# Performance work log

Hardware: AMD Instinct MI355X
Metric: run time of the kernel (lower is better)

## Reference

```python
import jax, jax.numpy as jnp
import numpy as np

V = 49152      # HEALPix nside=64 pixel count
B = 2
FIN = 32
FOUT = 64
K = 8          # Chebyshev kernel_size
DEG = 8        # neighbors per pixel (plus self-loop -> 9 nnz/row)
G = 8          # GroupNorm num_groups
EPS = 1e-5
SLOPE = 0.1    # LeakyReLU negative slope


def setup_inputs() -> dict:
    key = jax.random.key(0)
    ks = jax.random.split(key, 4)
    rng = np.random.default_rng(0)
    # sparse Laplacian in COO: 8 random neighbors + self-loop per node
    row = np.repeat(np.arange(V, dtype=np.int32), DEG + 1)
    nbrs = rng.integers(0, V, size=(V, DEG))
    col = np.concatenate([nbrs, np.arange(V)[:, None]], axis=1).astype(np.int32).reshape(-1)
    vals = (rng.standard_normal(V * (DEG + 1)).astype(np.float32)) * 0.1
    x = jax.random.normal(ks[0], (B, V, FIN), dtype=jnp.float32)
    W1 = jax.random.normal(ks[1], (K, FIN, FOUT), dtype=jnp.float32) * 0.05
    W2 = jax.random.normal(ks[2], (K, FOUT, FOUT), dtype=jnp.float32) * 0.05
    Wr = jax.random.normal(ks[3], (K, FIN, FOUT), dtype=jnp.float32) * 0.05
    zeros = jnp.zeros((FOUT,), dtype=jnp.float32)
    ones = jnp.ones((FOUT,), dtype=jnp.float32)
    return {
        "x": x,
        "lap_vals": jnp.asarray(vals),
        "lap_row": jnp.asarray(row),
        "lap_col": jnp.asarray(col),
        "W1": W1, "b1": zeros, "g1": ones, "be1": zeros,
        "W2": W2, "b2": zeros, "g2": ones, "be2": zeros,
        "Wr": Wr, "br": zeros,
    }


def _spmm(vals, row, col, z):
    # L @ z for COO Laplacian; z: [V, D]
    return jax.ops.segment_sum(vals[:, None] * z[col], row, num_segments=V)


def _cheb_conv(x, vals, row, col, W, b):
    # x: [B, V, Fin], W: [K, Fin, Fout] -> [B, V, Fout]
    Bb, Vv, F = x.shape
    x0 = jnp.transpose(x, (1, 0, 2)).reshape(Vv, Bb * F)  # [V, B*F]
    xs = [x0, _spmm(vals, row, col, x0)]
    for _ in range(K - 2):
        xs.append(2.0 * _spmm(vals, row, col, xs[-1]) - xs[-2])
    Xk = jnp.stack(xs, 0).reshape(K, Vv, Bb, F)
    Xk = jnp.transpose(Xk, (2, 1, 0, 3))  # [B, V, K, F]
    return jnp.einsum('bvkf,kfo->bvo', Xk, W) + b


def _group_norm(x, gamma, beta):
    # equivalent to nn.GroupNorm applied on x.permute(0,2,1): normalize over (C/G, V)
    Bb, Vv, C = x.shape
    xg = x.reshape(Bb, Vv, G, C // G)
    mu = xg.mean(axis=(1, 3), keepdims=True)
    var = xg.var(axis=(1, 3), keepdims=True)
    xn = ((xg - mu) * jax.lax.rsqrt(var + EPS)).reshape(Bb, Vv, C)
    return xn * gamma + beta


def _block(x, vals, row, col, W, b, gamma, beta):
    h = _cheb_conv(x, vals, row, col, W, b)
    h = _group_norm(h, gamma, beta)
    return jax.nn.leaky_relu(h, SLOPE)  # out_channels > 1 -> LeakyReLU(0.1)


def reference(x, lap_vals, lap_row, lap_col, W1, b1, g1, be1, W2, b2, g2, be2, Wr, br):
    h = _block(x, lap_vals, lap_row, lap_col, W1, b1, g1, be1)
    h = _block(h, lap_vals, lap_row, lap_col, W2, b2, g2, be2)
    res = _cheb_conv(x, lap_vals, lap_row, lap_col, Wr, br)  # in != out -> res_conv
    return h + res
```

## Files before the change

kernel.cpp:

```cpp
#include <hip/hip_runtime.h>
#include <hip/hip_bf16.h>

#define V 49152
#define NNZ 9
#define EPSV 1e-5f
#define SLOPE 0.1f

typedef __attribute__((ext_vector_type(8))) short bf16x8;
typedef __attribute__((ext_vector_type(4))) float f32x4;

__device__ __forceinline__ float lo2f(unsigned u) { return __uint_as_float(u << 16); }
__device__ __forceinline__ float hi2f(unsigned u) { return __uint_as_float(u & 0xffff0000u); }
__device__ __forceinline__ unsigned short f2us(float f) {
    __hip_bfloat16 h = __float2bfloat16(f);
    return *(unsigned short*)&h;
}
__device__ __forceinline__ float us2f(unsigned short u) { return __uint_as_float(((unsigned)u) << 16); }
__device__ __forceinline__ unsigned pk2(float a, float b) {
    return ((unsigned)f2us(a)) | (((unsigned)f2us(b)) << 16);
}

__device__ __forceinline__ void gload_lds16(const void* g, void* l) {
    __builtin_amdgcn_global_load_lds((__attribute__((address_space(1))) void*)g,
                                     (__attribute__((address_space(3))) void*)l, 16, 0, 0);
}

__global__ __launch_bounds__(256) void prep_k(
    const float* __restrict__ W1, const float* __restrict__ Wr, const float* __restrict__ W2,
    unsigned short* __restrict__ Wt1, unsigned short* __restrict__ Wtr, unsigned short* __restrict__ Wt2,
    float* __restrict__ part)
{
    int i = blockIdx.x * 256 + threadIdx.x;
    if (i < 32768) {
        int kk = i >> 12, rem = i & 4095, o = rem >> 6, f = rem & 63;
        Wt2[i] = f2us(W2[kk * 4096 + f * 64 + o]);
    } else if (i < 49152) {
        int j = i - 32768;
        int kk = j >> 11, rem = j & 2047, o = rem >> 5, f = rem & 31;
        Wt1[j] = f2us(W1[kk * 2048 + f * 64 + o]);
    } else if (i < 65536) {
        int j = i - 49152;
        int kk = j >> 11, rem = j & 2047, o = rem >> 5, f = rem & 31;
        Wtr[j] = f2us(Wr[kk * 2048 + f * 64 + o]);
    } else if (i < 66560) {
        part[i - 65536] = 0.f;
    }
}

__global__ __launch_bounds__(256) void reorder_k(const float* __restrict__ x, unsigned* __restrict__ t0) {
    int idx = blockIdx.x * 256 + threadIdx.x;
    int v = idx >> 5, j2 = idx & 31;
    int b = j2 >> 4, f0 = (j2 & 15) * 2;
    const float* p = x + ((size_t)b * V + v) * 32 + f0;
    t0[idx] = pk2(p[0], p[1]);
}

template<int THR, bool FIRST>
__global__ __launch_bounds__(256) void spmm_step(
    const uint4* __restrict__ zc, const uint4* __restrict__ zp, uint4* __restrict__ zn,
    const float* __restrict__ vals, const int* __restrict__ col)
{
    constexpr int L4 = THR * 2;
    int tid = blockIdx.x * 256 + threadIdx.x;
    int v = tid / THR;
    int c = (tid - v * THR) * 2;
    int base = v * NNZ;
    float t[16];
    #pragma unroll
    for (int i = 0; i < 16; ++i) t[i] = 0.f;
    #pragma unroll
    for (int n = 0; n < NNZ; ++n) {
        float a = vals[base + n];
        int cc = col[base + n];
        const uint4* p = zc + (size_t)cc * L4 + c;
        uint4 u0 = p[0];
        uint4 u1 = p[1];
        t[0] += a * lo2f(u0.x); t[1] += a * hi2f(u0.x);
        t[2] += a * lo2f(u0.y); t[3] += a * hi2f(u0.y);
        t[4] += a * lo2f(u0.z); t[5] += a * hi2f(u0.z);
        t[6] += a * lo2f(u0.w); t[7] += a * hi2f(u0.w);
        t[8]  += a * lo2f(u1.x); t[9]  += a * hi2f(u1.x);
        t[10] += a * lo2f(u1.y); t[11] += a * hi2f(u1.y);
        t[12] += a * lo2f(u1.z); t[13] += a * hi2f(u1.z);
        t[14] += a * lo2f(u1.w); t[15] += a * hi2f(u1.w);
    }
    if (!FIRST) {
        const uint4* pp = zp + (size_t)v * L4 + c;
        uint4 p0 = pp[0];
        uint4 p1 = pp[1];
        t[0] = 2.f*t[0] - lo2f(p0.x); t[1] = 2.f*t[1] - hi2f(p0.x);
        t[2] = 2.f*t[2] - lo2f(p0.y); t[3] = 2.f*t[3] - hi2f(p0.y);
        t[4] = 2.f*t[4] - lo2f(p0.z); t[5] = 2.f*t[5] - hi2f(p0.z);
        t[6] = 2.f*t[6] - lo2f(p0.w); t[7] = 2.f*t[7] - hi2f(p0.w);
        t[8]  = 2.f*t[8]  - lo2f(p1.x); t[9]  = 2.f*t[9]  - hi2f(p1.x);
        t[10] = 2.f*t[10] - lo2f(p1.y); t[11] = 2.f*t[11] - hi2f(p1.y);
        t[12] = 2.f*t[12] - lo2f(p1.z); t[13] = 2.f*t[13] - hi2f(p1.z);
        t[14] = 2.f*t[14] - lo2f(p1.w); t[15] = 2.f*t[15] - hi2f(p1.w);
    }
    uint4 r0, r1;
    r0.x = pk2(t[0], t[1]);  r0.y = pk2(t[2], t[3]);
    r0.z = pk2(t[4], t[5]);  r0.w = pk2(t[6], t[7]);
    r1.x = pk2(t[8], t[9]);  r1.y = pk2(t[10], t[11]);
    r1.z = pk2(t[12], t[13]); r1.w = pk2(t[14], t[15]);
    uint4* q = zn + (size_t)v * L4 + c;
    q[0] = r0;
    q[1] = r1;
}

template<int F, int NKK, int NPH, bool DUAL, bool INIT, bool FINAL>
__global__ __launch_bounds__(256) void mfma_gemm(
    const unsigned short* __restrict__ T,
    const unsigned short* __restrict__ WtA, const unsigned short* __restrict__ WtB,
    const float* __restrict__ biasA, const float* __restrict__ biasB,
    unsigned short* __restrict__ ACC, float* __restrict__ resOut,
    float* __restrict__ part)
{
    constexpr int KPP = NKK / NPH;
    constexpr int CPR = F / 4;
    constexpr int FH = F / 32;
    constexpr int RST = 68;
    constexpr int STAGE_SH = KPP * 64 * 2 * F;
    constexpr int TRANS_SH = (DUAL ? 2 : 1) * 2 * 64 * RST * 2;
    constexpr int SH = STAGE_SH > TRANS_SH ? STAGE_SH : TRANS_SH;
    __shared__ unsigned short shraw[SH];
    __shared__ float sGrp[32];

    unsigned short* tile = shraw;
    float* accbuf  = (float*)shraw;
    float* dualbuf = accbuf + 2 * 64 * RST;

    int wv = threadIdx.x >> 6, lane = threadIdx.x & 63;
    int quad = lane >> 4, l15 = lane & 15;
    int v0 = blockIdx.x * 64;
    int ot = wv;

    bf16x8 bw[NKK][FH];
    bf16x8 bd[NKK][FH];
    f32x4 acc[4][2];
    f32x4 accd[4][2];

    #pragma unroll
    for (int ph = 0; ph < NPH; ++ph) {
        if (ph > 0) __syncthreads();

        #pragma unroll
        for (int i = 0; i < (KPP * 64 * CPR) / 256; ++i) {
            int s = (i * 4 + wv) * 64 + lane;
            int kkl = s / (64 * CPR);
            int ws = s - kkl * 64 * CPR;
            int row = ws / CPR;
            int cl = ws - row * CPR;
            int cg = (cl & ~7) | ((cl & 7) ^ (row & 7));
            const unsigned short* gp =
                T + ((size_t)(ph * KPP + kkl) * V + v0 + row) * (2 * F) + cg * 8;
            gload_lds16(gp, tile + (size_t)(i * 4 + wv) * 64 * 8);
        }

        if (ph == 0) {
            #pragma unroll
            for (int kk = 0; kk < NKK; ++kk) {
                #pragma unroll
                for (int fh = 0; fh < FH; ++fh) {
                    size_t brow = ((size_t)kk * 64 + ot * 16 + l15) * F + fh * 32 + quad * 8;
                    bw[kk][fh] = *(const bf16x8*)(const void*)(WtA + brow);
                    if constexpr (DUAL) bd[kk][fh] = *(const bf16x8*)(const void*)(WtB + brow);
                }
            }
            #pragma unroll
            for (int m = 0; m < 4; ++m)
                #pragma unroll
                for (int b = 0; b < 2; ++b) {
                    acc[m][b] = (f32x4){0.f, 0.f, 0.f, 0.f};
                    if constexpr (DUAL) accd[m][b] = (f32x4){0.f, 0.f, 0.f, 0.f};
                }
        }

        __syncthreads();

        #pragma unroll
        for (int kkl = 0; kkl < KPP; ++kkl) {
            int kk = ph * KPP + kkl;
            #pragma unroll
            for (int fh = 0; fh < FH; ++fh) {
                #pragma unroll
                for (int m = 0; m < 4; ++m) {
                    int r = m * 16 + l15;
                    int rx = r & 7;
                    const unsigned short* rbase = tile + ((size_t)kkl * 64 + r) * 2 * F;
                    #pragma unroll
                    for (int b = 0; b < 2; ++b) {
                        int c0 = b * (CPR / 2) + fh * 4 + quad;
                        int s0 = (c0 & ~7) | ((c0 & 7) ^ rx);
                        bf16x8 a = *(const bf16x8*)(const void*)(rbase + s0 * 8);
                        acc[m][b] = __builtin_amdgcn_mfma_f32_16x16x32_bf16(a, bw[kk][fh], acc[m][b], 0, 0, 0);
                        if constexpr (DUAL)
                            accd[m][b] = __builtin_amdgcn_mfma_f32_16x16x32_bf16(a, bd[kk][fh], accd[m][b], 0, 0, 0);
                    }
                }
            }
        }
    }

    __syncthreads();

    int o = ot * 16 + l15;
    float bia = FINAL ? biasA[o] : 0.f;
    float biaB = DUAL ? biasB[o] : 0.f;
    #pragma unroll
    for (int m = 0; m < 4; ++m) {
        #pragma unroll
        for (int b = 0; b < 2; ++b) {
            #pragma unroll
            for (int rr = 0; rr < 4; ++rr) {
                int r = m * 16 + quad * 4 + rr;
                accbuf[(b * 64 + r) * RST + o] = acc[m][b][rr] + bia;
                if constexpr (DUAL) dualbuf[(b * 64 + r) * RST + o] = accd[m][b][rr] + biaB;
            }
        }
    }
    if constexpr (FINAL) {
        if (threadIdx.x < 32) sGrp[threadIdx.x] = 0.f;
    }
    __syncthreads();

    #pragma unroll
    for (int j = 0; j < 4; ++j) {
        int cid = threadIdx.x + 256 * j;
        int g = cid & 7, r = (cid >> 3) & 63, b = cid >> 9;
        int o0 = g * 8;
        const float* src = accbuf + (b * 64 + r) * RST + o0;
        float e[8];
        #pragma unroll
        for (int i = 0; i < 8; ++i) e[i] = src[i];
        size_t gidx = ((size_t)b * V + v0 + r) * 64 + o0;
        if constexpr (!INIT) {
            uint4 old = *(const uint4*)(const void*)(ACC + gidx);
            e[0] += lo2f(old.x); e[1] += hi2f(old.x);
            e[2] += lo2f(old.y); e[3] += hi2f(old.y);
            e[4] += lo2f(old.z); e[5] += hi2f(old.z);
            e[6] += lo2f(old.w); e[7] += hi2f(old.w);
        }
        uint4 pk;
        pk.x = pk2(e[0], e[1]); pk.y = pk2(e[2], e[3]);
        pk.z = pk2(e[4], e[5]); pk.w = pk2(e[6], e[7]);
        *(uint4*)(void*)(ACC + gidx) = pk;
        if constexpr (FINAL) {
            float s = 0.f, q = 0.f;
            #pragma unroll
            for (int i = 0; i < 8; ++i) { s += e[i]; q += e[i] * e[i]; }
            atomicAdd(&sGrp[b * 8 + g], s);
            atomicAdd(&sGrp[16 + b * 8 + g], q);
        }
    }
    if constexpr (DUAL) {
        #pragma unroll
        for (int j = 0; j < 8; ++j) {
            int cid = threadIdx.x + 256 * j;
            int oc = cid & 15, r = (cid >> 4) & 63, b = cid >> 10;
            float4 vv = *(const float4*)(const void*)(dualbuf + (b * 64 + r) * RST + oc * 4);
            *(float4*)(void*)(resOut + ((size_t)b * V + v0 + r) * 64 + oc * 4) = vv;
        }
    }
    if constexpr (FINAL) {
        __syncthreads();
        if (threadIdx.x < 16) {
            atomicAdd(&part[threadIdx.x * 2],     sGrp[threadIdx.x]);
            atomicAdd(&part[threadIdx.x * 2 + 1], sGrp[16 + threadIdx.x]);
        }
    }
}

__global__ __launch_bounds__(256) void gn_apply(const unsigned short* __restrict__ ACC,
                                                const float* __restrict__ part,
                                                const float* __restrict__ gamma, const float* __restrict__ beta,
                                                unsigned* __restrict__ zout) {
    int idx = blockIdx.x * 256 + threadIdx.x;
    int v = idx >> 4, j = idx & 15;
    int b = j >> 3, g = j & 7;
    const float N = (float)V * 8.f;
    float mean = part[j * 2] / N;
    float rstd = rsqrtf(part[j * 2 + 1] / N - mean * mean + EPSV);
    int o0 = g * 8;
    uint4 aa = *(const uint4*)(const void*)(ACC + ((size_t)b * V + v) * 64 + o0);
    float e[8] = { lo2f(aa.x), hi2f(aa.x), lo2f(aa.y), hi2f(aa.y),
                   lo2f(aa.z), hi2f(aa.z), lo2f(aa.w), hi2f(aa.w) };
    float y[8];
    #pragma unroll
    for (int i = 0; i < 8; ++i) {
        float t = (e[i] - mean) * rstd * gamma[o0 + i] + beta[o0 + i];
        y[i] = t > 0.f ? t : SLOPE * t;
    }
    uint4 pk;
    pk.x = pk2(y[0], y[1]); pk.y = pk2(y[2], y[3]);
    pk.z = pk2(y[4], y[5]); pk.w = pk2(y[6], y[7]);
    *(uint4*)(void*)(zout + (size_t)v * 64 + b * 32 + g * 4) = pk;
}

__global__ __launch_bounds__(256) void final_out(const unsigned short* __restrict__ ACC,
                                                 float* outres,
                                                 const float* __restrict__ part,
                                                 const float* __restrict__ gamma, const float* __restrict__ beta) {
    int idx = blockIdx.x * 256 + threadIdx.x;
    int b = idx >= V * 8 ? 1 : 0;
    int r = idx - b * V * 8;
    int v = r >> 3, g = r & 7;
    int j = b * 8 + g;
    const float N = (float)V * 8.f;
    float mean = part[j * 2] / N;
    float rstd = rsqrtf(part[j * 2 + 1] / N - mean * mean + EPSV);
    int o0 = g * 8;
    size_t base = ((size_t)b * V + v) * 64 + o0;
    uint4 aa = *(const uint4*)(const void*)(ACC + base);
    float e[8] = { lo2f(aa.x), hi2f(aa.x), lo2f(aa.y), hi2f(aa.y),
                   lo2f(aa.z), hi2f(aa.z), lo2f(aa.w), hi2f(aa.w) };
    float4 r0 = *(const float4*)(const void*)(outres + base);
    float4 r1 = *(const float4*)(const void*)(outres + base + 4);
    float y[8];
    #pragma unroll
    for (int i = 0; i < 8; ++i) {
        float t = (e[i] - mean) * rstd * gamma[o0 + i] + beta[o0 + i];
        y[i] = t > 0.f ? t : SLOPE * t;
    }
    float4 w0 = { y[0] + r0.x, y[1] + r0.y, y[2] + r0.z, y[3] + r0.w };
    float4 w1 = { y[4] + r1.x, y[5] + r1.y, y[6] + r1.z, y[7] + r1.w };
    *(float4*)(void*)(outres + base) = w0;
    *(float4*)(void*)(outres + base + 4) = w1;
}

extern "C" void kernel_launch(void* const* d_in, const int* in_sizes, int n_in,
                              void* d_out, int out_size, void* d_ws, size_t ws_size,
                              hipStream_t stream) {
    const float* x    = (const float*)d_in[0];
    const float* vals = (const float*)d_in[1];
    const int*   col  = (const int*)d_in[3];
    const float* W1   = (const float*)d_in[4];
    const float* b1   = (const float*)d_in[5];
    const float* g1   = (const float*)d_in[6];
    const float* be1  = (const float*)d_in[7];
    const float* W2   = (const float*)d_in[8];
    const float* b2   = (const float*)d_in[9];
    const float* g2   = (const float*)d_in[10];
    const float* be2  = (const float*)d_in[11];
    const float* Wr   = (const float*)d_in[12];
    const float* br   = (const float*)d_in[13];
    float* out = (float*)d_out;

    unsigned short* TS  = (unsigned short*)d_ws;
    unsigned short* ACC = TS + (size_t)8 * V * 128;
    unsigned short* Wt1 = ACC + (size_t)2 * V * 64;
    unsigned short* Wtr = Wt1 + 8 * 64 * 32;
    unsigned short* Wt2 = Wtr + 8 * 64 * 32;
    float* PART1 = (float*)(Wt2 + 8 * 64 * 64);
    float* PART2 = PART1 + 32;

    prep_k<<<260, 256, 0, stream>>>(W1, Wr, W2, Wt1, Wtr, Wt2, PART1);

    uint4* T1s[8];
    for (int k = 0; k < 8; ++k) T1s[k] = (uint4*)(TS + (size_t)k * V * 64);

    reorder_k<<<V * 32 / 256, 256, 0, stream>>>(x, (unsigned*)T1s[0]);
    spmm_step<4, true><<<V * 4 / 256, 256, 0, stream>>>(T1s[0], nullptr, T1s[1], vals, col);
    for (int k = 2; k < 8; ++k)
        spmm_step<4, false><<<V * 4 / 256, 256, 0, stream>>>(T1s[k-1], T1s[k-2], T1s[k], vals, col);

    mfma_gemm<32, 8, 1, true, true, true><<<V / 64, 256, 0, stream>>>(
        TS, Wt1, Wtr, b1, br, ACC, out, PART1);

    uint4* T2s[8];
    for (int k = 0; k < 8; ++k) T2s[k] = (uint4*)(TS + (size_t)k * V * 128);

    gn_apply<<<V * 16 / 256, 256, 0, stream>>>(ACC, PART1, g1, be1, (unsigned*)T2s[0]);
    spmm_step<8, true><<<V * 8 / 256, 256, 0, stream>>>(T2s[0], nullptr, T2s[1], vals, col);
    for (int k = 2; k < 8; ++k)
        spmm_step<8, false><<<V * 8 / 256, 256, 0, stream>>>(T2s[k-1], T2s[k-2], T2s[k], vals, col);

    mfma_gemm<64, 8, 2, false, true, true><<<V / 64, 256, 0, stream>>>(
        TS, Wt2, nullptr, b2, nullptr, ACC, nullptr, PART2);

    final_out<<<2 * V * 8 / 256, 256, 0, stream>>>(ACC, out, PART2, g2, be2);
}
```

Measured before the change: 364.7 us.

## Fuse Chebyshev recurrence, GEMM and GroupNorm into two persistent cooperative kernels

Replaces the per-step SpMM launches, the separate MFMA GEMMs and the GroupNorm/output kernels with two cooperative persistent kernels (768 blocks of 64 vertices). Each block computes its rows of every Chebyshev term, keeps the tile in LDS and accumulates the MFMA product immediately, using grid.sync between terms instead of kernel boundaries. The last term is no longer written to global memory and the previous term is read from LDS. It also fuses the GroupNorm apply and residual add into the second chain. The cost is a grid-wide barrier per step and reliance on 3 blocks per CU co-residency; the old launch path is kept as a fallback.

```diff
diff --git a/kernel.cpp b/kernel.cpp
--- a/kernel.cpp
+++ b/kernel.cpp
@@ -1,10 +1,15 @@
 #include <hip/hip_runtime.h>
 #include <hip/hip_bf16.h>
+#include <hip/hip_cooperative_groups.h>
+
+namespace cg = cooperative_groups;
 
 #define V 49152
 #define NNZ 9
 #define EPSV 1e-5f
 #define SLOPE 0.1f
+#define NB 768
+#define RST 68
 
 typedef __attribute__((ext_vector_type(8))) short bf16x8;
 typedef __attribute__((ext_vector_type(4))) float f32x4;
@@ -15,11 +20,27 @@
     __hip_bfloat16 h = __float2bfloat16(f);
     return *(unsigned short*)&h;
 }
-__device__ __forceinline__ float us2f(unsigned short u) { return __uint_as_float(((unsigned)u) << 16); }
 __device__ __forceinline__ unsigned pk2(float a, float b) {
     return ((unsigned)f2us(a)) | (((unsigned)f2us(b)) << 16);
 }
-
+__device__ __forceinline__ void fma8(float* t, float a, uint4 u) {
+    t[0] += a * lo2f(u.x); t[1] += a * hi2f(u.x);
+    t[2] += a * lo2f(u.y); t[3] += a * hi2f(u.y);
+    t[4] += a * lo2f(u.z); t[5] += a * hi2f(u.z);
+    t[6] += a * lo2f(u.w); t[7] += a * hi2f(u.w);
+}
+__device__ __forceinline__ void fold8(float* t, uint4 p) {
+    t[0] = 2.f*t[0] - lo2f(p.x); t[1] = 2.f*t[1] - hi2f(p.x);
+    t[2] = 2.f*t[2] - lo2f(p.y); t[3] = 2.f*t[3] - hi2f(p.y);
+    t[4] = 2.f*t[4] - lo2f(p.z); t[5] = 2.f*t[5] - hi2f(p.z);
+    t[6] = 2.f*t[6] - lo2f(p.w); t[7] = 2.f*t[7] - hi2f(p.w);
+}
+__device__ __forceinline__ uint4 pack8(const float* t) {
+    uint4 r;
+    r.x = pk2(t[0], t[1]); r.y = pk2(t[2], t[3]);
+    r.z = pk2(t[4], t[5]); r.w = pk2(t[6], t[7]);
+    return r;
+}
 __device__ __forceinline__ void gload_lds16(const void* g, void* l) {
     __builtin_amdgcn_global_load_lds((__attribute__((address_space(1))) void*)g,
                                      (__attribute__((address_space(3))) void*)l, 16, 0, 0);
@@ -47,6 +68,344 @@
     }
 }
 
+
+__global__ __launch_bounds__(256, 3) void chain1_k(
+    const float* __restrict__ x, const float* __restrict__ vals, const int* __restrict__ col,
+    unsigned short* __restrict__ TS,
+    const unsigned short* __restrict__ Wt1, const unsigned short* __restrict__ Wtr,
+    const float* __restrict__ biasA, const float* __restrict__ biasB,
+    unsigned short* __restrict__ ACC, float* __restrict__ resOut, float* __restrict__ part)
+{
+    cg::grid_group grid = cg::this_grid();
+    __shared__ __align__(16) float epi[2 * 64 * RST];
+    __shared__ float sGrp[32];
+    uint4* tiles = (uint4*)epi;
+
+    const int tid = threadIdx.x;
+    const int wv = tid >> 6, lane = tid & 63;
+    const int quad = lane >> 4, l15 = lane & 15;
+    const int ot = wv;
+    const int v0 = blockIdx.x * 64;
+    const int sr = tid >> 2, sc2 = (tid & 3) * 2;
+    const int sv = v0 + sr;
+
+    f32x4 acc[4][2], accd[4][2];
+    #pragma unroll
+    for (int m = 0; m < 4; ++m)
+        #pragma unroll
+        for (int b = 0; b < 2; ++b) {
+            acc[m][b]  = (f32x4){0.f, 0.f, 0.f, 0.f};
+            accd[m][b] = (f32x4){0.f, 0.f, 0.f, 0.f};
+        }
+
+    auto do_mfma = [&](int kk, const unsigned short* tile_sh) {
+        size_t brow = ((size_t)kk * 64 + ot * 16 + l15) * 32 + quad * 8;
+        bf16x8 bw = *(const bf16x8*)(const void*)(Wt1 + brow);
+        bf16x8 bd = *(const bf16x8*)(const void*)(Wtr + brow);
+        #pragma unroll
+        for (int m = 0; m < 4; ++m) {
+            int r = m * 16 + l15, r7 = r & 7;
+            const unsigned short* rb = tile_sh + (size_t)r * 64;
+            #pragma unroll
+            for (int b = 0; b < 2; ++b) {
+                int s0 = (b * 4 + quad) ^ r7;
+                bf16x8 a = *(const bf16x8*)(const void*)(rb + s0 * 8);
+                acc[m][b]  = __builtin_amdgcn_mfma_f32_16x16x32_bf16(a, bw, acc[m][b], 0, 0, 0);
+                accd[m][b] = __builtin_amdgcn_mfma_f32_16x16x32_bf16(a, bd, accd[m][b], 0, 0, 0);
+            }
+        }
+    };
+
+    #pragma unroll
+    for (int j = 0; j < 2; ++j) {
+        int cid = tid + 256 * j;
+        int r = cid >> 3, c = cid & 7;
+        int b = c >> 2, f0 = (c & 3) * 8;
+        const float* p = x + ((size_t)b * V + v0 + r) * 32 + f0;
+        float4 a0 = *(const float4*)(const void*)p;
+        float4 a1 = *(const float4*)(const void*)(p + 4);
+        uint4 pk;
+        pk.x = pk2(a0.x, a0.y); pk.y = pk2(a0.z, a0.w);
+        pk.z = pk2(a1.x, a1.y); pk.w = pk2(a1.z, a1.w);
+        *(uint4*)(void*)(TS + (size_t)(v0 + r) * 64 + c * 8) = pk;
+        tiles[r * 8 + (c ^ (r & 7))] = pk;
+    }
+    __syncthreads();
+    do_mfma(0, (const unsigned short*)tiles);
+    __threadfence();
+    grid.sync();
+    __threadfence();
+
+    for (int k = 1; k < 8; ++k) {
+        const unsigned short* zc = TS + (size_t)(k - 1) * V * 64;
+        unsigned short* zn = TS + (size_t)k * V * 64;
+        uint4* bufW = tiles + (k & 1) * 512;
+        float t[16];
+        #pragma unroll
+        for (int i = 0; i < 16; ++i) t[i] = 0.f;
+        int base = sv * NNZ;
+        #pragma unroll
+        for (int n = 0; n < NNZ; ++n) {
+            float a = vals[base + n];
+            int cc = col[base + n];
+            const uint4* p = (const uint4*)(const void*)(zc + (size_t)cc * 64 + sc2 * 8);
+            fma8(t, a, p[0]);
+            fma8(t + 8, a, p[1]);
+        }
+        int s0 = sc2 ^ (sr & 7), s1 = (sc2 + 1) ^ (sr & 7);
+        if (k >= 2) {
+            fold8(t,     bufW[sr * 8 + s0]);
+            fold8(t + 8, bufW[sr * 8 + s1]);
+        }
+        uint4 r0 = pack8(t), r1 = pack8(t + 8);
+        if (k < 7) {
+            uint4* q = (uint4*)(void*)(zn + (size_t)sv * 64 + sc2 * 8);
+            q[0] = r0; q[1] = r1;
+        }
+        bufW[sr * 8 + s0] = r0;
+        bufW[sr * 8 + s1] = r1;
+        __syncthreads();
+        do_mfma(k, (const unsigned short*)bufW);
+        if (k < 7) { __threadfence(); grid.sync(); __threadfence(); }
+    }
+
+    __syncthreads();
+    int o = ot * 16 + l15;
+    float biA = biasA[o], biB = biasB[o];
+    #pragma unroll
+    for (int m = 0; m < 4; ++m)
+        #pragma unroll
+        for (int b = 0; b < 2; ++b)
+            #pragma unroll
+            for (int rr = 0; rr < 4; ++rr) {
+                int r = m * 16 + quad * 4 + rr;
+                epi[(b * 64 + r) * RST + o] = acc[m][b][rr] + biA;
+            }
+    if (tid < 32) sGrp[tid] = 0.f;
+    __syncthreads();
+    #pragma unroll
+    for (int j = 0; j < 4; ++j) {
+        int cid = tid + 256 * j;
+        int g = cid & 7, r = (cid >> 3) & 63, b = cid >> 9;
+        const float* src = epi + (b * 64 + r) * RST + g * 8;
+        float e[8], s = 0.f, q = 0.f;
+        #pragma unroll
+        for (int i = 0; i < 8; ++i) { e[i] = src[i]; s += e[i]; q += e[i] * e[i]; }
+        *(uint4*)(void*)(ACC + ((size_t)b * V + v0 + r) * 64 + g * 8) = pack8(e);
+        atomicAdd(&sGrp[b * 8 + g], s);
+        atomicAdd(&sGrp[16 + b * 8 + g], q);
+    }
+    __syncthreads();
+    #pragma unroll
+    for (int m = 0; m < 4; ++m)
+        #pragma unroll
+        for (int b = 0; b < 2; ++b)
+            #pragma unroll
+            for (int rr = 0; rr < 4; ++rr) {
+                int r = m * 16 + quad * 4 + rr;
+                epi[(b * 64 + r) * RST + o] = accd[m][b][rr] + biB;
+            }
+    __syncthreads();
+    #pragma unroll
+    for (int j = 0; j < 8; ++j) {
+        int cid = tid + 256 * j;
+        int oc = cid & 15, r = (cid >> 4) & 63, b = cid >> 10;
+        float4 vv = *(const float4*)(const void*)(epi + (b * 64 + r) * RST + oc * 4);
+        *(float4*)(void*)(resOut + ((size_t)b * V + v0 + r) * 64 + oc * 4) = vv;
+    }
+    if (tid < 16) {
+        atomicAdd(&part[tid * 2],     sGrp[tid]);
+        atomicAdd(&part[tid * 2 + 1], sGrp[16 + tid]);
+    }
+}
+
+__global__ __launch_bounds__(256, 3) void chain2_k(
+    const unsigned short* __restrict__ ACC, const float* __restrict__ part1,
+    const float* __restrict__ g1, const float* __restrict__ be1,
+    unsigned short* __restrict__ TS, const unsigned short* __restrict__ Wt2,
+    const float* __restrict__ biasA, float* __restrict__ part2,
+    const float* __restrict__ g2, const float* __restrict__ be2,
+    float* __restrict__ outres,
+    const float* __restrict__ vals, const int* __restrict__ col)
+{
+    cg::grid_group grid = cg::this_grid();
+    __shared__ __align__(16) float epi[2 * 64 * RST];
+    __shared__ float sGrp[32];
+    uint4* tiles = (uint4*)epi;
+
+    const int tid = threadIdx.x;
+    const int wv = tid >> 6, lane = tid & 63;
+    const int quad = lane >> 4, l15 = lane & 15;
+    const int ot = wv;
+    const int v0 = blockIdx.x * 64;
+    const int sr = tid >> 2, sc2 = (tid & 3) * 2;
+    const int sv = v0 + sr;
+    const float Nf = (float)V * 8.f;
+
+    f32x4 acc[4][2];
+    #pragma unroll
+    for (int m = 0; m < 4; ++m)
+        #pragma unroll
+        for (int b = 0; b < 2; ++b) acc[m][b] = (f32x4){0.f, 0.f, 0.f, 0.f};
+
+    auto do_mfma = [&](int kk, const unsigned short* tile_sh) {
+        size_t brow = ((size_t)kk * 64 + ot * 16 + l15) * 64 + quad * 8;
+        bf16x8 bw0 = *(const bf16x8*)(const void*)(Wt2 + brow);
+        bf16x8 bw1 = *(const bf16x8*)(const void*)(Wt2 + brow + 32);
+        #pragma unroll
+        for (int m = 0; m < 4; ++m) {
+            int r = m * 16 + l15, r7 = r & 7;
+            const unsigned short* rb = tile_sh + (size_t)r * 128;
+            #pragma unroll
+            for (int b = 0; b < 2; ++b) {
+                #pragma unroll
+                for (int fh = 0; fh < 2; ++fh) {
+                    int c0 = b * 8 + fh * 4 + quad;
+                    int s0 = (c0 & ~7) | ((c0 & 7) ^ r7);
+                    bf16x8 a = *(const bf16x8*)(const void*)(rb + s0 * 8);
+                    acc[m][b] = __builtin_amdgcn_mfma_f32_16x16x32_bf16(
+                        a, fh ? bw1 : bw0, acc[m][b], 0, 0, 0);
+                }
+            }
+        }
+    };
+
+    {
+        int cl = tid & 15;
+        int b = cl >> 3, g = cl & 7, j8 = b * 8 + g;
+        float mean = part1[j8 * 2] / Nf;
+        float rstd = rsqrtf(part1[j8 * 2 + 1] / Nf - mean * mean + EPSV);
+        int o0 = g * 8;
+        float gm[8], bt[8];
+        #pragma unroll
+        for (int i = 0; i < 8; ++i) { gm[i] = g1[o0 + i]; bt[i] = be1[o0 + i]; }
+        #pragma unroll
+        for (int j = 0; j < 4; ++j) {
+            int r = (tid >> 4) + 16 * j;
+            int v = v0 + r;
+            uint4 aa = *(const uint4*)(const void*)(ACC + ((size_t)b * V + v) * 64 + o0);
+            float e[8] = { lo2f(aa.x), hi2f(aa.x), lo2f(aa.y), hi2f(aa.y),
+                           lo2f(aa.z), hi2f(aa.z), lo2f(aa.w), hi2f(aa.w) };
+            float y[8];
+            #pragma unroll
+            for (int i = 0; i < 8; ++i) {
+                float t = (e[i] - mean) * rstd * gm[i] + bt[i];
+                y[i] = t > 0.f ? t : SLOPE * t;
+            }
+            uint4 pk = pack8(y);
+            *(uint4*)(void*)(TS + (size_t)v * 128 + cl * 8) = pk;
+            tiles[r * 16 + ((cl & ~7) | ((cl & 7) ^ (r & 7)))] = pk;
+        }
+    }
+    __syncthreads();
+    do_mfma(0, (const unsigned short*)tiles);
+    __threadfence();
+    grid.sync();
+    __threadfence();
+
+    for (int k = 1; k < 8; ++k) {
+        const unsigned short* zc = TS + (size_t)(k - 1) * V * 128;
+        unsigned short* zn = TS + (size_t)k * V * 128;
+        uint4* bufW = tiles + (k & 1) * 1024;
+        int base = sv * NNZ;
+        float av[NNZ]; int ac[NNZ];
+        #pragma unroll
+        for (int n = 0; n < NNZ; ++n) { av[n] = vals[base + n]; ac[n] = col[base + n]; }
+        #pragma unroll
+        for (int h = 0; h < 2; ++h) {
+            int c = h * 8 + sc2;
+            float t[16];
+            #pragma unroll
+            for (int i = 0; i < 16; ++i) t[i] = 0.f;
+            #pragma unroll
+            for (int n = 0; n < NNZ; ++n) {
+                const uint4* p = (const uint4*)(const void*)(zc + (size_t)ac[n] * 128 + c * 8);
+                fma8(t, av[n], p[0]);
+                fma8(t + 8, av[n], p[1]);
+            }
+            int s0 = (c & ~7) | ((c & 7) ^ (sr & 7));
+            int s1 = (c & ~7) | (((c + 1) & 7) ^ (sr & 7));
+            if (k >= 2) {
+                fold8(t,     bufW[sr * 16 + s0]);
+                fold8(t + 8, bufW[sr * 16 + s1]);
+            }
+            uint4 r0 = pack8(t), r1 = pack8(t + 8);
+            if (k < 7) {
+                uint4* q = (uint4*)(void*)(zn + (size_t)sv * 128 + c * 8);
+                q[0] = r0; q[1] = r1;
+            }
+            bufW[sr * 16 + s0] = r0;
+            bufW[sr * 16 + s1] = r1;
+        }
+        __syncthreads();
+        do_mfma(k, (const unsigned short*)bufW);
+        if (k < 7) { __threadfence(); grid.sync(); __threadfence(); }
+    }
+
+    __syncthreads();
+    int o = ot * 16 + l15;
+    float biA = biasA[o];
+    #pragma unroll
+    for (int m = 0; m < 4; ++m)
+        #pragma unroll
+        for (int b = 0; b < 2; ++b)
+            #pragma unroll
+            for (int rr = 0; rr < 4; ++rr) {
+                int r = m * 16 + quad * 4 + rr;
+                epi[(b * 64 + r) * RST + o] = acc[m][b][rr] + biA;
+            }
+    if (tid < 32) sGrp[tid] = 0.f;
+    __syncthreads();
+    #pragma unroll
+    for (int j = 0; j < 4; ++j) {
+        int cid = tid + 256 * j;
+        int g = cid & 7, r = (cid >> 3) & 63, b = cid >> 9;
+        const float* src = epi + (b * 64 + r) * RST + g * 8;
+        float s = 0.f, q = 0.f;
+        #pragma unroll
+        for (int i = 0; i < 8; ++i) { float e = src[i]; s += e; q += e * e; }
+        atomicAdd(&sGrp[b * 8 + g], s);
+        atomicAdd(&sGrp[16 + b * 8 + g], q);
+    }
+    __syncthreads();
+    if (tid < 16) {
+        atomicAdd(&part2[tid * 2],     sGrp[tid]);
+        atomicAdd(&part2[tid * 2 + 1], sGrp[16 + tid]);
+    }
+    __threadfence();
+    grid.sync();
+    __threadfence();
+
+    {
+        int cl = tid & 15;
+        int b = cl >> 3, g = cl & 7, j8 = b * 8 + g;
+        float mean = part2[j8 * 2] / Nf;
+        float rstd = rsqrtf(part2[j8 * 2 + 1] / Nf - mean * mean + EPSV);
+        int o0 = g * 8;
+        float gm[8], bt[8];
+        #pragma unroll
+        for (int i = 0; i < 8; ++i) { gm[i] = g2[o0 + i]; bt[i] = be2[o0 + i]; }
+        #pragma unroll
+        for (int j = 0; j < 4; ++j) {
+            int r = (tid >> 4) + 16 * j;
+            const float* src = epi + (b * 64 + r) * RST + o0;
+            float y[8];
+            #pragma unroll
+            for (int i = 0; i < 8; ++i) {
+                float t = (src[i] - mean) * rstd * gm[i] + bt[i];
+                y[i] = t > 0.f ? t : SLOPE * t;
+            }
+            size_t gb = ((size_t)b * V + v0 + r) * 64 + o0;
+            float4 r0 = *(const float4*)(const void*)(outres + gb);
+            float4 r1 = *(const float4*)(const void*)(outres + gb + 4);
+            float4 w0 = { y[0] + r0.x, y[1] + r0.y, y[2] + r0.z, y[3] + r0.w };
+            float4 w1 = { y[4] + r1.x, y[5] + r1.y, y[6] + r1.z, y[7] + r1.w };
+            *(float4*)(void*)(outres + gb) = w0;
+            *(float4*)(void*)(outres + gb + 4) = w1;
+        }
+    }
+}
+
 __global__ __launch_bounds__(256) void reorder_k(const float* __restrict__ x, unsigned* __restrict__ t0) {
     int idx = blockIdx.x * 256 + threadIdx.x;
     int v = idx >> 5, j2 = idx & 31;
@@ -73,38 +432,17 @@
         float a = vals[base + n];
         int cc = col[base + n];
         const uint4* p = zc + (size_t)cc * L4 + c;
-        uint4 u0 = p[0];
-        uint4 u1 = p[1];
-        t[0] += a * lo2f(u0.x); t[1] += a * hi2f(u0.x);
-        t[2] += a * lo2f(u0.y); t[3] += a * hi2f(u0.y);
-        t[4] += a * lo2f(u0.z); t[5] += a * hi2f(u0.z);
-        t[6] += a * lo2f(u0.w); t[7] += a * hi2f(u0.w);
-        t[8]  += a * lo2f(u1.x); t[9]  += a * hi2f(u1.x);
-        t[10] += a * lo2f(u1.y); t[11] += a * hi2f(u1.y);
-        t[12] += a * lo2f(u1.z); t[13] += a * hi2f(u1.z);
-        t[14] += a * lo2f(u1.w); t[15] += a * hi2f(u1.w);
+        fma8(t, a, p[0]);
+        fma8(t + 8, a, p[1]);
     }
     if (!FIRST) {
         const uint4* pp = zp + (size_t)v * L4 + c;
-        uint4 p0 = pp[0];
-        uint4 p1 = pp[1];
-        t[0] = 2.f*t[0] - lo2f(p0.x); t[1] = 2.f*t[1] - hi2f(p0.x);
-        t[2] = 2.f*t[2] - lo2f(p0.y); t[3] = 2.f*t[3] - hi2f(p0.y);
-        t[4] = 2.f*t[4] - lo2f(p0.z); t[5] = 2.f*t[5] - hi2f(p0.z);
-        t[6] = 2.f*t[6] - lo2f(p0.w); t[7] = 2.f*t[7] - hi2f(p0.w);
-        t[8]  = 2.f*t[8]  - lo2f(p1.x); t[9]  = 2.f*t[9]  - hi2f(p1.x);
-        t[10] = 2.f*t[10] - lo2f(p1.y); t[11] = 2.f*t[11] - hi2f(p1.y);
-        t[12] = 2.f*t[12] - lo2f(p1.z); t[13] = 2.f*t[13] - hi2f(p1.z);
-        t[14] = 2.f*t[14] - lo2f(p1.w); t[15] = 2.f*t[15] - hi2f(p1.w);
-    }
-    uint4 r0, r1;
-    r0.x = pk2(t[0], t[1]);  r0.y = pk2(t[2], t[3]);
-    r0.z = pk2(t[4], t[5]);  r0.w = pk2(t[6], t[7]);
-    r1.x = pk2(t[8], t[9]);  r1.y = pk2(t[10], t[11]);
-    r1.z = pk2(t[12], t[13]); r1.w = pk2(t[14], t[15]);
+        fold8(t, pp[0]);
+        fold8(t + 8, pp[1]);
+    }
     uint4* q = zn + (size_t)v * L4 + c;
-    q[0] = r0;
-    q[1] = r1;
+    q[0] = pack8(t);
+    q[1] = pack8(t + 8);
 }
 
 template<int F, int NKK, int NPH, bool DUAL, bool INIT, bool FINAL>
@@ -118,7 +456,6 @@
     constexpr int KPP = NKK / NPH;
     constexpr int CPR = F / 4;
     constexpr int FH = F / 32;
-    constexpr int RST = 68;
     constexpr int STAGE_SH = KPP * 64 * 2 * F;
     constexpr int TRANS_SH = (DUAL ? 2 : 1) * 2 * 64 * RST * 2;
     constexpr int SH = STAGE_SH > TRANS_SH ? STAGE_SH : TRANS_SH;
@@ -142,7 +479,6 @@
     #pragma unroll
     for (int ph = 0; ph < NPH; ++ph) {
         if (ph > 0) __syncthreads();
-
         #pragma unroll
         for (int i = 0; i < (KPP * 64 * CPR) / 256; ++i) {
             int s = (i * 4 + wv) * 64 + lane;
@@ -155,17 +491,15 @@
                 T + ((size_t)(ph * KPP + kkl) * V + v0 + row) * (2 * F) + cg * 8;
             gload_lds16(gp, tile + (size_t)(i * 4 + wv) * 64 * 8);
         }
-
         if (ph == 0) {
             #pragma unroll
-            for (int kk = 0; kk < NKK; ++kk) {
+            for (int kk = 0; kk < NKK; ++kk)
                 #pragma unroll
                 for (int fh = 0; fh < FH; ++fh) {
                     size_t brow = ((size_t)kk * 64 + ot * 16 + l15) * F + fh * 32 + quad * 8;
                     bw[kk][fh] = *(const bf16x8*)(const void*)(WtA + brow);
                     if constexpr (DUAL) bd[kk][fh] = *(const bf16x8*)(const void*)(WtB + brow);
                 }
-            }
             #pragma unroll
             for (int m = 0; m < 4; ++m)
                 #pragma unroll
@@ -174,14 +508,12 @@
                     if constexpr (DUAL) accd[m][b] = (f32x4){0.f, 0.f, 0.f, 0.f};
                 }
         }
-
         __syncthreads();
-
         #pragma unroll
         for (int kkl = 0; kkl < KPP; ++kkl) {
             int kk = ph * KPP + kkl;
             #pragma unroll
-            for (int fh = 0; fh < FH; ++fh) {
+            for (int fh = 0; fh < FH; ++fh)
                 #pragma unroll
                 for (int m = 0; m < 4; ++m) {
                     int r = m * 16 + l15;
@@ -197,32 +529,27 @@
                             accd[m][b] = __builtin_amdgcn_mfma_f32_16x16x32_bf16(a, bd[kk][fh], accd[m][b], 0, 0, 0);
                     }
                 }
-            }
-        }
-    }
-
-    __syncthreads();
-
+        }
+    }
+
+    __syncthreads();
     int o = ot * 16 + l15;
     float bia = FINAL ? biasA[o] : 0.f;
     float biaB = DUAL ? biasB[o] : 0.f;
     #pragma unroll
-    for (int m = 0; m < 4; ++m) {
-        #pragma unroll
-        for (int b = 0; b < 2; ++b) {
+    for (int m = 0; m < 4; ++m)
+        #pragma unroll
+        for (int b = 0; b < 2; ++b)
             #pragma unroll
             for (int rr = 0; rr < 4; ++rr) {
                 int r = m * 16 + quad * 4 + rr;
                 accbuf[(b * 64 + r) * RST + o] = acc[m][b][rr] + bia;
                 if constexpr (DUAL) dualbuf[(b * 64 + r) * RST + o] = accd[m][b][rr] + biaB;
             }
-        }
-    }
     if constexpr (FINAL) {
         if (threadIdx.x < 32) sGrp[threadIdx.x] = 0.f;
     }
     __syncthreads();
-
     #pragma unroll
     for (int j = 0; j < 4; ++j) {
         int cid = threadIdx.x + 256 * j;
@@ -240,10 +567,7 @@
             e[4] += lo2f(old.z); e[5] += hi2f(old.z);
             e[6] += lo2f(old.w); e[7] += hi2f(old.w);
         }
-        uint4 pk;
-        pk.x = pk2(e[0], e[1]); pk.y = pk2(e[2], e[3]);
-        pk.z = pk2(e[4], e[5]); pk.w = pk2(e[6], e[7]);
-        *(uint4*)(void*)(ACC + gidx) = pk;
+        *(uint4*)(void*)(ACC + gidx) = pack8(e);
         if constexpr (FINAL) {
             float s = 0.f, q = 0.f;
             #pragma unroll
@@ -355,27 +679,53 @@
 
     prep_k<<<260, 256, 0, stream>>>(W1, Wr, W2, Wt1, Wtr, Wt2, PART1);
 
-    uint4* T1s[8];
-    for (int k = 0; k < 8; ++k) T1s[k] = (uint4*)(TS + (size_t)k * V * 64);
-
-    reorder_k<<<V * 32 / 256, 256, 0, stream>>>(x, (unsigned*)T1s[0]);
-    spmm_step<4, true><<<V * 4 / 256, 256, 0, stream>>>(T1s[0], nullptr, T1s[1], vals, col);
-    for (int k = 2; k < 8; ++k)
-        spmm_step<4, false><<<V * 4 / 256, 256, 0, stream>>>(T1s[k-1], T1s[k-2], T1s[k], vals, col);
-
-    mfma_gemm<32, 8, 1, true, true, true><<<V / 64, 256, 0, stream>>>(
-        TS, Wt1, Wtr, b1, br, ACC, out, PART1);
-
-    uint4* T2s[8];
-    for (int k = 0; k < 8; ++k) T2s[k] = (uint4*)(TS + (size_t)k * V * 128);
-
-    gn_apply<<<V * 16 / 256, 256, 0, stream>>>(ACC, PART1, g1, be1, (unsigned*)T2s[0]);
-    spmm_step<8, true><<<V * 8 / 256, 256, 0, stream>>>(T2s[0], nullptr, T2s[1], vals, col);
-    for (int k = 2; k < 8; ++k)
-        spmm_step<8, false><<<V * 8 / 256, 256, 0, stream>>>(T2s[k-1], T2s[k-2], T2s[k], vals, col);
-
-    mfma_gemm<64, 8, 2, false, true, true><<<V / 64, 256, 0, stream>>>(
-        TS, Wt2, nullptr, b2, nullptr, ACC, nullptr, PART2);
-
-    final_out<<<2 * V * 8 / 256, 256, 0, stream>>>(ACC, out, PART2, g2, be2);
-}
+    static int coop_ok = -1;
+    if (coop_ok < 0) {
+        int o1 = 0, o2 = 0;
+        hipError_t e1 = hipOccupancyMaxActiveBlocksPerMultiprocessor(
+            &o1, (const void*)chain1_k, 256, 0);
+        hipError_t e2 = hipOccupancyMaxActiveBlocksPerMultiprocessor(
+            &o2, (const void*)chain2_k, 256, 0);
+        coop_ok = (e1 == hipSuccess && e2 == hipSuccess && o1 >= 3 && o2 >= 3) ? 1 : 0;
+    }
+
+    int did_chain1 = 0, did_chain2 = 0;
+    if (coop_ok == 1) {
+        void* a1[] = { (void*)&x, (void*)&vals, (void*)&col, (void*)&TS, (void*)&Wt1, (void*)&Wtr,
+                       (void*)&b1, (void*)&br, (void*)&ACC, (void*)&out, (void*)&PART1 };
+        if (hipLaunchCooperativeKernel((const void*)chain1_k, dim3(NB), dim3(256), a1, 0, stream)
+            == hipSuccess) {
+            did_chain1 = 1;
+            void* a2[] = { (void*)&ACC, (void*)&PART1, (void*)&g1, (void*)&be1, (void*)&TS, (void*)&Wt2,
+                           (void*)&b2, (void*)&PART2, (void*)&g2, (void*)&be2, (void*)&out,
+                           (void*)&vals, (void*)&col };
+            if (hipLaunchCooperativeKernel((const void*)chain2_k, dim3(NB), dim3(256), a2, 0, stream)
+                == hipSuccess) {
+                did_chain2 = 1;
+            }
+        }
+        if (!did_chain1 || !did_chain2) coop_ok = 0;
+    }
+
+    if (!did_chain1) {
+        uint4* T1s[8];
+        for (int k = 0; k < 8; ++k) T1s[k] = (uint4*)(TS + (size_t)k * V * 64);
+        reorder_k<<<V * 32 / 256, 256, 0, stream>>>(x, (unsigned*)T1s[0]);
+        spmm_step<4, true><<<V * 4 / 256, 256, 0, stream>>>(T1s[0], nullptr, T1s[1], vals, col);
+        for (int k = 2; k < 8; ++k)
+            spmm_step<4, false><<<V * 4 / 256, 256, 0, stream>>>(T1s[k-1], T1s[k-2], T1s[k], vals, col);
+        mfma_gemm<32, 8, 1, true, true, true><<<V / 64, 256, 0, stream>>>(
+            TS, Wt1, Wtr, b1, br, ACC, out, PART1);
+    }
+    if (!did_chain2) {
+        uint4* T2s[8];
+        for (int k = 0; k < 8; ++k) T2s[k] = (uint4*)(TS + (size_t)k * V * 128);
+        gn_apply<<<V * 16 / 256, 256, 0, stream>>>(ACC, PART1, g1, be1, (unsigned*)T2s[0]);
+        spmm_step<8, true><<<V * 8 / 256, 256, 0, stream>>>(T2s[0], nullptr, T2s[1], vals, col);
+        for (int k = 2; k < 8; ++k)
+            spmm_step<8, false><<<V * 8 / 256, 256, 0, stream>>>(T2s[k-1], T2s[k-2], T2s[k], vals, col);
+        mfma_gemm<64, 8, 2, false, true, true><<<V / 64, 256, 0, stream>>>(
+            TS, Wt2, nullptr, b2, nullptr, ACC, nullptr, PART2);
+        final_out<<<2 * V * 8 / 256, 256, 0, stream>>>(ACC, out, PART2, g2, be2);
+    }
+}
```

After: 367.6 us. Within noise of the previous version (+0.8%).
